# Kernel optimization log

Measured on AMD Instinct MI355X. Metric: run time of the kernel, lower is better.

Reference implementation:

```python
import jax, jax.numpy as jnp
import numpy as np

NUM_HEADS = 8
WEIGHTS_DIM = 512
INPUT_DIM = 512
D_HEAD = WEIGHTS_DIM // NUM_HEADS


def setup_inputs() -> dict:
    key = jax.random.key(0)
    ks = jax.random.split(key, 9)
    B, S, D = 4, 2048, INPUT_DIM
    s_in = 1.0 / np.sqrt(D)
    s_w = 1.0 / np.sqrt(WEIGHTS_DIM)
    return {
        "x": jax.random.normal(ks[0], (B, S, D), dtype=jnp.float32),
        "Wq": jax.random.normal(ks[1], (D, WEIGHTS_DIM), dtype=jnp.float32) * s_in,
        "bq": jnp.zeros((WEIGHTS_DIM,), dtype=jnp.float32),
        "Wk": jax.random.normal(ks[2], (D, WEIGHTS_DIM), dtype=jnp.float32) * s_in,
        "bk": jnp.zeros((WEIGHTS_DIM,), dtype=jnp.float32),
        "Wv": jax.random.normal(ks[3], (D, WEIGHTS_DIM), dtype=jnp.float32) * s_in,
        "bv": jnp.zeros((WEIGHTS_DIM,), dtype=jnp.float32),
        "Wh": jax.random.normal(ks[4], (WEIGHTS_DIM, D), dtype=jnp.float32) * s_w,
        "bh": jnp.zeros((D,), dtype=jnp.float32),
    }


def _split_heads(t):
    # [B, S, Dm] -> [B, H, S, d_head]
    B, S, _ = t.shape
    return t.reshape(B, S, NUM_HEADS, D_HEAD).transpose(0, 2, 1, 3)


def reference(x, Wq, bq, Wk, bk, Wv, bv, Wh, bh):
    q = _split_heads(x @ Wq + bq)
    k = _split_heads(x @ Wk + bk)
    v = _split_heads(x @ Wv + bv)
    scale = 1.0 / jnp.sqrt(jnp.float32(D_HEAD))
    scores = jnp.einsum("bhqd,bhkd->bhqk", q, k) * scale  # [B,H,S,S]
    weights = jax.nn.softmax(scores, axis=-1)
    attn = jnp.einsum("bhqk,bhkd->bhqd", weights, v)
    B, H, S, d = attn.shape
    concat = attn.transpose(0, 2, 1, 3).reshape(B, S, H * d)
    return concat @ Wh + bh
```

## Files before the change

kernel.cpp:

```cpp
#include <hip/hip_runtime.h>
#include <stdint.h>

#define NB  4
#define SS  2048
#define DD  512
#define HH  8
#define DHH 64
#define MM  (NB * SS)

typedef __attribute__((ext_vector_type(8))) short bf16x8;
typedef __attribute__((ext_vector_type(4))) float f32x4;
typedef __attribute__((ext_vector_type(4))) short s16x4;

union fu32 { float f; unsigned u; };
union pfu  { uint4 u; bf16x8 v; };

static __device__ __forceinline__ short f2bf(float f) {
  fu32 a; a.f = f;
  unsigned u = a.u;
  return (short)((u + 0x7fffu + ((u >> 16) & 1u)) >> 16);
}
static __device__ __forceinline__ float bf2f(short s) {
  fu32 t; t.u = ((unsigned)(unsigned short)s) << 16;
  return t.f;
}

static __device__ __forceinline__ void async16(const void* g, void* l) {
  __builtin_amdgcn_global_load_lds(
      (__attribute__((address_space(1))) unsigned*)(void*)g,
      (__attribute__((address_space(3))) unsigned*)l, 16, 0, 0);
}

__global__ __launch_bounds__(256) void prep_kernel(
    const float* __restrict__ x, short* __restrict__ xb,
    const float* __restrict__ W0, const float* __restrict__ W1,
    const float* __restrict__ W2, const float* __restrict__ W3,
    short* __restrict__ T0, short* __restrict__ T1,
    short* __restrict__ T2, short* __restrict__ T3) {
  const int bid = blockIdx.x, tid = threadIdx.x;
  if (bid < 2048) {
    int i = (bid * 256 + tid) * 8;
    float4 v0 = *(const float4*)(x + i);
    float4 v1 = *(const float4*)(x + i + 4);
    bf16x8 o;
    o[0] = f2bf(v0.x); o[1] = f2bf(v0.y); o[2] = f2bf(v0.z); o[3] = f2bf(v0.w);
    o[4] = f2bf(v1.x); o[5] = f2bf(v1.y); o[6] = f2bf(v1.z); o[7] = f2bf(v1.w);
    *(bf16x8*)(xb + i) = o;
  } else {
    int z = bid - 2048;
    int widx = z >> 6, rem = z & 63;
    const float* W = widx == 0 ? W0 : widx == 1 ? W1 : widx == 2 ? W2 : W3;
    short*       T = widx == 0 ? T0 : widx == 1 ? T1 : widx == 2 ? T2 : T3;
    int n  = (rem & 7) * 64 + (tid & 63);
    int k0 = (rem >> 3) * 64 + (tid >> 6) * 16;
    bf16x8 t0, t1;
#pragma unroll
    for (int j = 0; j < 8; ++j) t0[j] = f2bf(W[(size_t)(k0 + j) * DD + n]);
#pragma unroll
    for (int j = 0; j < 8; ++j) t1[j] = f2bf(W[(size_t)(k0 + 8 + j) * DD + n]);
    *(bf16x8*)(T + (size_t)n * DD + k0)     = t0;
    *(bf16x8*)(T + (size_t)n * DD + k0 + 8) = t1;
  }
}

__global__ __launch_bounds__(256, 4) void gemm_qkv_kernel(
    const short* __restrict__ A, const short* __restrict__ Bt,
    const float* __restrict__ bq, const float* __restrict__ bk,
    const float* __restrict__ bv, short* __restrict__ qout,
    short* __restrict__ kout, short* __restrict__ vtout, float qscale) {
  __shared__ __align__(16) short a_sh[64 * 64];
  __shared__ __align__(16) short b_sh[128 * 64];
  const int tid  = threadIdx.x;
  const int w    = tid >> 6, lane = tid & 63, quad = lane >> 4, l16 = lane & 15;
  const int m0   = blockIdx.y * 64, n0 = blockIdx.x * 128;
  const int mw   = (w >> 1) * 32,   nw = (w & 1) * 64;
  const int rw   = lane >> 3, seg = lane & 7, gs = seg ^ rw;
  const int sxz  = l16 & 7;

  f32x4 acc[2][4];
#pragma unroll
  for (int i = 0; i < 2; ++i)
#pragma unroll
    for (int j = 0; j < 4; ++j) acc[i][j] = {0.f, 0.f, 0.f, 0.f};

  for (int kt = 0; kt < DD; kt += 64) {
    __syncthreads();
    {
      const short* ga = A  + (size_t)(m0 + w * 16 + rw) * DD + kt + gs * 8;
      const short* gb = Bt + (size_t)(n0 + w * 32 + rw) * DD + kt + gs * 8;
#pragma unroll
      for (int i = 0; i < 2; ++i)
        async16(ga + (size_t)i * 8 * DD, &a_sh[(w * 16 + i * 8) * 64]);
#pragma unroll
      for (int i = 0; i < 4; ++i)
        async16(gb + (size_t)i * 8 * DD, &b_sh[(w * 32 + i * 8) * 64]);
    }
    __syncthreads();
#pragma unroll
    for (int ks = 0; ks < 2; ++ks) {
      const int so = ((ks * 4 + quad) ^ sxz) * 8;
      bf16x8 af[2], bfr[4];
#pragma unroll
      for (int mt = 0; mt < 2; ++mt)
        af[mt] = *(const bf16x8*)&a_sh[(mw + mt * 16 + l16) * 64 + so];
#pragma unroll
      for (int nt = 0; nt < 4; ++nt)
        bfr[nt] = *(const bf16x8*)&b_sh[(nw + nt * 16 + l16) * 64 + so];
#pragma unroll
      for (int mt = 0; mt < 2; ++mt)
#pragma unroll
        for (int nt = 0; nt < 4; ++nt)
          acc[mt][nt] = __builtin_amdgcn_mfma_f32_16x16x32_bf16(
              af[mt], bfr[nt], acc[mt][nt], 0, 0, 0);
    }
  }

#pragma unroll
  for (int nt = 0; nt < 4; ++nt) {
    const int n   = n0 + nw + nt * 16 + l16;
    const int sg  = n >> 9, n9 = n & 511, h = n9 >> 6, d = n & 63;
    const float bval = (sg == 0 ? bq : sg == 1 ? bk : bv)[n9];
    const float scl  = (sg == 0) ? qscale : 1.0f;
#pragma unroll
    for (int mt = 0; mt < 2; ++mt) {
      const int mb = m0 + mw + mt * 16 + quad * 4;
      const int bi = mb >> 11, s = mb & (SS - 1);
      if (sg == 2) {
        s16x4 pk;
#pragma unroll
        for (int r = 0; r < 4; ++r) pk[r] = f2bf(acc[mt][nt][r] + bval);
        *(s16x4*)&vtout[((size_t)(bi * HH + h) * DHH + d) * SS + s] = pk;
      } else {
        short* o = (sg == 0) ? qout : kout;
        const size_t base = ((size_t)(bi * HH + h) * SS + s) * DHH + d;
#pragma unroll
        for (int r = 0; r < 4; ++r)
          o[base + (size_t)r * DHH] = f2bf((acc[mt][nt][r] + bval) * scl);
      }
    }
  }
}

__global__ __launch_bounds__(256, 4) void attn_kernel(
    const short* __restrict__ Qa, const short* __restrict__ Ka,
    const short* __restrict__ Vt, short* __restrict__ Op0,
    short* __restrict__ Op1, float* __restrict__ lpw) {
  __shared__ __align__(16) short k_sh[128 * 64];
  __shared__ __align__(16) short vt_sh[64 * 128];

  const int tid  = threadIdx.x;
  const int w    = tid >> 6, lane = tid & 63, quad = lane >> 4, l16 = lane & 15;
  const int n    = blockIdx.x;
  const int grp  = (n & 7) * 8 + (n >> 7);
  const int qt_b = (n >> 3) & 15;
  const int half = grp & 1, h = (grp >> 1) & 7, b = grp >> 4;
  const int q0   = qt_b * 128;
  const int rw = lane >> 3, seg = lane & 7, gs = seg ^ rw;
  const int sxz = l16 & 7;
  const size_t base = (size_t)(b * HH + h) * SS * DHH;
  const short* Qg = Qa + base + (size_t)(q0 + w * 32) * DHH;
  const short* Kg = Ka + base;
  const short* Vg = Vt + base;

  bf16x8 qf[2][2];
#pragma unroll
  for (int mt = 0; mt < 2; ++mt)
#pragma unroll
    for (int ks = 0; ks < 2; ++ks)
      qf[mt][ks] = *(const bf16x8*)(Qg + (size_t)(mt * 16 + l16) * DHH + ks * 32 + quad * 8);

  bf16x8 ones;
#pragma unroll
  for (int j = 0; j < 8; ++j) ones[j] = (short)0x3F80;

  f32x4 o_acc[2][4];
#pragma unroll
  for (int qt = 0; qt < 2; ++qt)
#pragma unroll
    for (int dt = 0; dt < 4; ++dt) o_acc[qt][dt] = {0.f, 0.f, 0.f, 0.f};
  f32x4 l_acc[2] = {{0.f, 0.f, 0.f, 0.f}, {0.f, 0.f, 0.f, 0.f}};

  const int addrA = ((((quad & 1) << 1) + (quad >> 1)) * 16 + l16) * 4;
  const int addrB = addrA ^ 64;
  const bool qeven = (quad & 1) == 0;

  const int kstart = half * (SS / 2);

  for (int kb = kstart; kb < kstart + SS / 2; kb += 128) {
    __syncthreads();
    {
      const short* gk = Kg + (size_t)(kb + w * 32 + rw) * DHH + gs * 8;
#pragma unroll
      for (int i = 0; i < 4; ++i)
        async16(gk + (size_t)i * 8 * DHH, &k_sh[(w * 32 + i * 8) * 64]);
#pragma unroll
      for (int i = 0; i < 4; ++i) {
        const int d = w * 16 + i * 4 + (lane >> 4);
        const int gseg = (lane & 15) ^ (d & 15);
        async16(Vg + (size_t)d * SS + kb + gseg * 8,
                &vt_sh[(w * 16 + i * 4) * 128]);
      }
    }
    __syncthreads();

#pragma unroll
    for (int ck = 0; ck < 4; ++ck) {
      uint2 pk[2][2];
#pragma unroll
      for (int t = 0; t < 2; ++t) {
        const int knt = ck * 2 + t;
        bf16x8 kf0 = *(const bf16x8*)&k_sh[(knt * 16 + l16) * 64 + ((0 * 4 + quad) ^ sxz) * 8];
        bf16x8 kf1 = *(const bf16x8*)&k_sh[(knt * 16 + l16) * 64 + ((1 * 4 + quad) ^ sxz) * 8];
#pragma unroll
        for (int qt = 0; qt < 2; ++qt) {
          f32x4 s = {0.f, 0.f, 0.f, 0.f};
          s = __builtin_amdgcn_mfma_f32_16x16x32_bf16(kf0, qf[qt][0], s, 0, 0, 0);
          s = __builtin_amdgcn_mfma_f32_16x16x32_bf16(kf1, qf[qt][1], s, 0, 0, 0);
          fu32 e0, e1, e2, e3;
          e0.f = __builtin_amdgcn_exp2f(s[0]);
          e1.f = __builtin_amdgcn_exp2f(s[1]);
          e2.f = __builtin_amdgcn_exp2f(s[2]);
          e3.f = __builtin_amdgcn_exp2f(s[3]);
          pk[qt][t].x = __builtin_amdgcn_perm(e1.u, e0.u, 0x07060302u);
          pk[qt][t].y = __builtin_amdgcn_perm(e3.u, e2.u, 0x07060302u);
        }
      }
      pfu pf[2];
#pragma unroll
      for (int qt = 0; qt < 2; ++qt) {
        unsigned p1x = (unsigned)__shfl_xor((int)pk[qt][1].x, 16);
        unsigned p1y = (unsigned)__shfl_xor((int)pk[qt][1].y, 16);
        unsigned v0x = qeven ? pk[qt][0].x : p1x;
        unsigned v0y = qeven ? pk[qt][0].y : p1y;
        unsigned v2x = qeven ? p1x : pk[qt][0].x;
        unsigned v2y = qeven ? p1y : pk[qt][0].y;
        pf[qt].u.x = (unsigned)__builtin_amdgcn_ds_bpermute(addrA, (int)v0x);
        pf[qt].u.y = (unsigned)__builtin_amdgcn_ds_bpermute(addrA, (int)v0y);
        pf[qt].u.z = (unsigned)__builtin_amdgcn_ds_bpermute(addrB, (int)v2x);
        pf[qt].u.w = (unsigned)__builtin_amdgcn_ds_bpermute(addrB, (int)v2y);
        l_acc[qt] = __builtin_amdgcn_mfma_f32_16x16x32_bf16(pf[qt].v, ones, l_acc[qt], 0, 0, 0);
      }
#pragma unroll
      for (int dt = 0; dt < 4; ++dt) {
        bf16x8 vf = *(const bf16x8*)&vt_sh[(dt * 16 + l16) * 128 + ((ck * 4 + quad) ^ l16) * 8];
        o_acc[0][dt] = __builtin_amdgcn_mfma_f32_16x16x32_bf16(pf[0].v, vf, o_acc[0][dt], 0, 0, 0);
        o_acc[1][dt] = __builtin_amdgcn_mfma_f32_16x16x32_bf16(pf[1].v, vf, o_acc[1][dt], 0, 0, 0);
      }
    }
  }

  short* Op = half ? Op1 : Op0;
#pragma unroll
  for (int qt = 0; qt < 2; ++qt) {
#pragma unroll
    for (int r = 0; r < 4; ++r) {
      const int qg = q0 + w * 32 + qt * 16 + quad * 4 + r;
      const size_t row = (size_t)(b * HH + h) * SS + qg;
      if (l16 == 0)
        lpw[(size_t)half * (NB * HH * SS) + row] = l_acc[qt][r];
      const float inv = __builtin_amdgcn_rcpf(l_acc[qt][r]);
#pragma unroll
      for (int dt = 0; dt < 4; ++dt)
        Op[row * DHH + dt * 16 + l16] = f2bf(o_acc[qt][dt][r] * inv);
    }
  }
}

__global__ void attn_combine_kernel(const short* __restrict__ Op0,
                                    const short* __restrict__ Op1,
                                    const float* __restrict__ lpw,
                                    short* __restrict__ aws) {
  int idx  = blockIdx.x * 256 + threadIdx.x;
  int dsg  = idx & 7;
  int row  = idx >> 3;
  int q    = row & (SS - 1);
  int bh   = row >> 11, h = bh & 7, b = bh >> 3;
  float l1 = lpw[row], l2 = lpw[NB * HH * SS + row];
  float inv = 1.f / (l1 + l2);
  float w1 = l1 * inv, w2 = l2 * inv;
  bf16x8 a = *(const bf16x8*)&Op0[(size_t)row * DHH + dsg * 8];
  bf16x8 c = *(const bf16x8*)&Op1[(size_t)row * DHH + dsg * 8];
  bf16x8 o;
#pragma unroll
  for (int j = 0; j < 8; ++j) o[j] = f2bf(w1 * bf2f(a[j]) + w2 * bf2f(c[j]));
  *(bf16x8*)&aws[((size_t)(b * SS + q)) * DD + h * DHH + dsg * 8] = o;
}

__global__ __launch_bounds__(256, 4) void gemm_proj_kernel(
    const short* __restrict__ A, const short* __restrict__ Bt,
    const float* __restrict__ bias, float* __restrict__ out) {
  __shared__ __align__(16) short a_sh[64 * 64];
  __shared__ __align__(16) short b_sh[64 * 64];
  const int tid = threadIdx.x;
  const int w   = tid >> 6, lane = tid & 63, quad = lane >> 4, l16 = lane & 15;
  const int m0  = blockIdx.y * 64, n0 = blockIdx.x * 64;
  const int mw  = (w >> 1) * 32, nw = (w & 1) * 32;
  const int rw  = lane >> 3, seg = lane & 7, gs = seg ^ rw;
  const int sxz = l16 & 7;

  f32x4 acc[2][2];
#pragma unroll
  for (int i = 0; i < 2; ++i)
#pragma unroll
    for (int j = 0; j < 2; ++j) acc[i][j] = {0.f, 0.f, 0.f, 0.f};

  for (int kt = 0; kt < DD; kt += 64) {
    __syncthreads();
    {
      const short* ga = A  + (size_t)(m0 + w * 16 + rw) * DD + kt + gs * 8;
      const short* gb = Bt + (size_t)(n0 + w * 16 + rw) * DD + kt + gs * 8;
#pragma unroll
      for (int i = 0; i < 2; ++i) {
        async16(ga + (size_t)i * 8 * DD, &a_sh[(w * 16 + i * 8) * 64]);
        async16(gb + (size_t)i * 8 * DD, &b_sh[(w * 16 + i * 8) * 64]);
      }
    }
    __syncthreads();
#pragma unroll
    for (int ks = 0; ks < 2; ++ks) {
      const int so = ((ks * 4 + quad) ^ sxz) * 8;
      bf16x8 af0 = *(const bf16x8*)&a_sh[(mw + l16) * 64 + so];
      bf16x8 af1 = *(const bf16x8*)&a_sh[(mw + 16 + l16) * 64 + so];
#pragma unroll
      for (int nt = 0; nt < 2; ++nt) {
        bf16x8 bfr = *(const bf16x8*)&b_sh[(nw + nt * 16 + l16) * 64 + so];
        acc[0][nt] = __builtin_amdgcn_mfma_f32_16x16x32_bf16(af0, bfr, acc[0][nt], 0, 0, 0);
        acc[1][nt] = __builtin_amdgcn_mfma_f32_16x16x32_bf16(af1, bfr, acc[1][nt], 0, 0, 0);
      }
    }
  }

#pragma unroll
  for (int nt = 0; nt < 2; ++nt) {
    const int   n  = n0 + nw + nt * 16 + l16;
    const float bv = bias[n];
#pragma unroll
    for (int mt = 0; mt < 2; ++mt)
#pragma unroll
      for (int r = 0; r < 4; ++r) {
        const int m = m0 + mw + mt * 16 + quad * 4 + r;
        out[(size_t)m * DD + n] = acc[mt][nt][r] + bv;
      }
  }
}

extern "C" void kernel_launch(void* const* d_in, const int* in_sizes, int n_in,
                              void* d_out, int out_size, void* d_ws, size_t ws_size,
                              hipStream_t stream) {
  (void)in_sizes; (void)n_in; (void)out_size; (void)ws_size;
  const float* x  = (const float*)d_in[0];
  const float* Wq = (const float*)d_in[1];
  const float* bq = (const float*)d_in[2];
  const float* Wk = (const float*)d_in[3];
  const float* bk = (const float*)d_in[4];
  const float* Wv = (const float*)d_in[5];
  const float* bv = (const float*)d_in[6];
  const float* Wh = (const float*)d_in[7];
  const float* bh = (const float*)d_in[8];

  short* ws  = (short*)d_ws;
  short* xb  = ws;
  short* wqt = xb  + (size_t)MM * DD;
  short* wkt = wqt + (size_t)DD * DD;
  short* wvt = wkt + (size_t)DD * DD;
  short* wht = wvt + (size_t)DD * DD;
  short* qws = wht + (size_t)DD * DD;
  short* kws = qws + (size_t)MM * DD;
  short* vws = kws + (size_t)MM * DD;
  short* aws = vws + (size_t)MM * DD;
  short* op1 = aws + (size_t)MM * DD;
  float* lpw = (float*)(op1 + (size_t)MM * DD);

  hipLaunchKernelGGL(prep_kernel, dim3(2048 + 256), dim3(256), 0, stream,
                     x, xb, Wq, Wk, Wv, Wh, wqt, wkt, wvt, wht);

  const float qscale = 1.4426950408889634f / 8.0f;
  hipLaunchKernelGGL(gemm_qkv_kernel, dim3(12, 128), dim3(256), 0, stream,
                     xb, wqt, bq, bk, bv, qws, kws, vws, qscale);

  hipLaunchKernelGGL(attn_kernel, dim3(1024), dim3(256), 0, stream,
                     qws, kws, vws, xb, op1, lpw);
  hipLaunchKernelGGL(attn_combine_kernel, dim3(NB * HH * SS * 8 / 256), dim3(256), 0, stream,
                     xb, op1, lpw, aws);

  hipLaunchKernelGGL(gemm_proj_kernel, dim3(8, 128), dim3(256), 0, stream,
                     aws, wht, bh, (float*)d_out);
}
```

Before: 176.1 us.

## Enlarge QKV GEMM tile and register-prefetch K/V tiles in attention

The QKV projection GEMM now uses 128x128 block tiles instead of 64x128, so each warp computes a 64x64 sub-tile. This halves the grid and increases reuse of each loaded A/B fragment, at the cost of more accumulator registers and a lower occupancy bound. The attention kernel replaces the async global-to-LDS copies with register prefetch of the next K/V tile, issued while the current tile is being computed, then stored to LDS at the top of the next iteration. This overlaps global memory latency with the MFMA work but raises register pressure.

```diff
diff --git a/kernel.cpp b/kernel.cpp
--- a/kernel.cpp
+++ b/kernel.cpp
@@ -63,34 +63,34 @@
   }
 }
 
-__global__ __launch_bounds__(256, 4) void gemm_qkv_kernel(
+__global__ __launch_bounds__(256, 3) void gemm_qkv_kernel(
     const short* __restrict__ A, const short* __restrict__ Bt,
     const float* __restrict__ bq, const float* __restrict__ bk,
     const float* __restrict__ bv, short* __restrict__ qout,
     short* __restrict__ kout, short* __restrict__ vtout, float qscale) {
-  __shared__ __align__(16) short a_sh[64 * 64];
+  __shared__ __align__(16) short a_sh[128 * 64];
   __shared__ __align__(16) short b_sh[128 * 64];
   const int tid  = threadIdx.x;
   const int w    = tid >> 6, lane = tid & 63, quad = lane >> 4, l16 = lane & 15;
-  const int m0   = blockIdx.y * 64, n0 = blockIdx.x * 128;
-  const int mw   = (w >> 1) * 32,   nw = (w & 1) * 64;
+  const int m0   = blockIdx.y * 128, n0 = blockIdx.x * 128;
+  const int mw   = (w >> 1) * 64,    nw = (w & 1) * 64;
   const int rw   = lane >> 3, seg = lane & 7, gs = seg ^ rw;
   const int sxz  = l16 & 7;
 
-  f32x4 acc[2][4];
-#pragma unroll
-  for (int i = 0; i < 2; ++i)
+  f32x4 acc[4][4];
+#pragma unroll
+  for (int i = 0; i < 4; ++i)
 #pragma unroll
     for (int j = 0; j < 4; ++j) acc[i][j] = {0.f, 0.f, 0.f, 0.f};
 
   for (int kt = 0; kt < DD; kt += 64) {
     __syncthreads();
     {
-      const short* ga = A  + (size_t)(m0 + w * 16 + rw) * DD + kt + gs * 8;
+      const short* ga = A  + (size_t)(m0 + w * 32 + rw) * DD + kt + gs * 8;
       const short* gb = Bt + (size_t)(n0 + w * 32 + rw) * DD + kt + gs * 8;
 #pragma unroll
-      for (int i = 0; i < 2; ++i)
-        async16(ga + (size_t)i * 8 * DD, &a_sh[(w * 16 + i * 8) * 64]);
+      for (int i = 0; i < 4; ++i)
+        async16(ga + (size_t)i * 8 * DD, &a_sh[(w * 32 + i * 8) * 64]);
 #pragma unroll
       for (int i = 0; i < 4; ++i)
         async16(gb + (size_t)i * 8 * DD, &b_sh[(w * 32 + i * 8) * 64]);
@@ -99,15 +99,15 @@
 #pragma unroll
     for (int ks = 0; ks < 2; ++ks) {
       const int so = ((ks * 4 + quad) ^ sxz) * 8;
-      bf16x8 af[2], bfr[4];
-#pragma unroll
-      for (int mt = 0; mt < 2; ++mt)
+      bf16x8 af[4], bfr[4];
+#pragma unroll
+      for (int mt = 0; mt < 4; ++mt)
         af[mt] = *(const bf16x8*)&a_sh[(mw + mt * 16 + l16) * 64 + so];
 #pragma unroll
       for (int nt = 0; nt < 4; ++nt)
         bfr[nt] = *(const bf16x8*)&b_sh[(nw + nt * 16 + l16) * 64 + so];
 #pragma unroll
-      for (int mt = 0; mt < 2; ++mt)
+      for (int mt = 0; mt < 4; ++mt)
 #pragma unroll
         for (int nt = 0; nt < 4; ++nt)
           acc[mt][nt] = __builtin_amdgcn_mfma_f32_16x16x32_bf16(
@@ -122,7 +122,7 @@
     const float bval = (sg == 0 ? bq : sg == 1 ? bk : bv)[n9];
     const float scl  = (sg == 0) ? qscale : 1.0f;
 #pragma unroll
-    for (int mt = 0; mt < 2; ++mt) {
+    for (int mt = 0; mt < 4; ++mt) {
       const int mb = m0 + mw + mt * 16 + quad * 4;
       const int bi = mb >> 11, s = mb & (SS - 1);
       if (sg == 2) {
@@ -185,23 +185,42 @@
   const bool qeven = (quad & 1) == 0;
 
   const int kstart = half * (SS / 2);
-
-  for (int kb = kstart; kb < kstart + SS / 2; kb += 128) {
-    __syncthreads();
-    {
-      const short* gk = Kg + (size_t)(kb + w * 32 + rw) * DHH + gs * 8;
+  const int kend   = kstart + SS / 2;
+
+  const int vd0   = w * 16 + (lane >> 4);
+  uint4 kr[4], vr[4];
+#pragma unroll
+  for (int i = 0; i < 4; ++i)
+    kr[i] = *(const uint4*)(Kg + (size_t)(kstart + w * 32 + i * 8 + rw) * DHH + gs * 8);
+#pragma unroll
+  for (int i = 0; i < 4; ++i) {
+    const int d = vd0 + i * 4;
+    const int gseg = l16 ^ (d & 15);
+    vr[i] = *(const uint4*)(Vg + (size_t)d * SS + kstart + gseg * 8);
+  }
+
+  for (int kb = kstart; kb < kend; kb += 128) {
+    __syncthreads();
+#pragma unroll
+    for (int i = 0; i < 4; ++i)
+      *(uint4*)((char*)&k_sh[(w * 32 + i * 8) * 64] + lane * 16) = kr[i];
+#pragma unroll
+    for (int i = 0; i < 4; ++i)
+      *(uint4*)((char*)&vt_sh[(w * 16 + i * 4) * 128] + lane * 16) = vr[i];
+    __syncthreads();
+
+    if (kb + 128 < kend) {
+      const int nkb = kb + 128;
 #pragma unroll
       for (int i = 0; i < 4; ++i)
-        async16(gk + (size_t)i * 8 * DHH, &k_sh[(w * 32 + i * 8) * 64]);
+        kr[i] = *(const uint4*)(Kg + (size_t)(nkb + w * 32 + i * 8 + rw) * DHH + gs * 8);
 #pragma unroll
       for (int i = 0; i < 4; ++i) {
-        const int d = w * 16 + i * 4 + (lane >> 4);
-        const int gseg = (lane & 15) ^ (d & 15);
-        async16(Vg + (size_t)d * SS + kb + gseg * 8,
-                &vt_sh[(w * 16 + i * 4) * 128]);
-      }
-    }
-    __syncthreads();
+        const int d = vd0 + i * 4;
+        const int gseg = l16 ^ (d & 15);
+        vr[i] = *(const uint4*)(Vg + (size_t)d * SS + nkb + gseg * 8);
+      }
+    }
 
 #pragma unroll
     for (int ck = 0; ck < 4; ++ck) {
@@ -375,7 +394,7 @@
                      x, xb, Wq, Wk, Wv, Wh, wqt, wkt, wvt, wht);
 
   const float qscale = 1.4426950408889634f / 8.0f;
-  hipLaunchKernelGGL(gemm_qkv_kernel, dim3(12, 128), dim3(256), 0, stream,
+  hipLaunchKernelGGL(gemm_qkv_kernel, dim3(12, 64), dim3(256), 0, stream,
                      xb, wqt, bq, bk, bv, qws, kws, vws, qscale);
 
   hipLaunchKernelGGL(attn_kernel, dim3(1024), dim3(256), 0, stream,
```

After: 231.7 us. +31.6%, slower.

## Double-buffer K/V tiles in attention kernel with 64-key stages

Applied to the files above, without the earlier changes.

Replaces the single 128-key K/Vt shared-memory tile with two 64-key buffers, so the async copy of the next tile is issued before computing on the current one. This removes one barrier per iteration and lets global loads overlap with the MFMA work. The tile is halved, so there are twice as many iterations, and the V swizzle changes to match the narrower layout. Total LDS use stays the same.

```diff
diff --git a/kernel.cpp b/kernel.cpp
--- a/kernel.cpp
+++ b/kernel.cpp
@@ -145,8 +145,8 @@
     const short* __restrict__ Qa, const short* __restrict__ Ka,
     const short* __restrict__ Vt, short* __restrict__ Op0,
     short* __restrict__ Op1, float* __restrict__ lpw) {
-  __shared__ __align__(16) short k_sh[128 * 64];
-  __shared__ __align__(16) short vt_sh[64 * 128];
+  __shared__ __align__(16) short k_sh[2][64 * 64];
+  __shared__ __align__(16) short vt_sh[2][64 * 64];
 
   const int tid  = threadIdx.x;
   const int w    = tid >> 6, lane = tid & 63, quad = lane >> 4, l16 = lane & 15;
@@ -185,32 +185,36 @@
   const bool qeven = (quad & 1) == 0;
 
   const int kstart = half * (SS / 2);
-
-  for (int kb = kstart; kb < kstart + SS / 2; kb += 128) {
-    __syncthreads();
-    {
-      const short* gk = Kg + (size_t)(kb + w * 32 + rw) * DHH + gs * 8;
-#pragma unroll
-      for (int i = 0; i < 4; ++i)
-        async16(gk + (size_t)i * 8 * DHH, &k_sh[(w * 32 + i * 8) * 64]);
-#pragma unroll
-      for (int i = 0; i < 4; ++i) {
-        const int d = w * 16 + i * 4 + (lane >> 4);
-        const int gseg = (lane & 15) ^ (d & 15);
-        async16(Vg + (size_t)d * SS + kb + gseg * 8,
-                &vt_sh[(w * 16 + i * 4) * 128]);
-      }
-    }
-    __syncthreads();
-
-#pragma unroll
-    for (int ck = 0; ck < 4; ++ck) {
+  const int kend   = kstart + SS / 2;
+
+  auto stage = [&](int bsel, int kb) {
+    const short* gk = Kg + (size_t)(kb + w * 16 + rw) * DHH + gs * 8;
+#pragma unroll
+    for (int i = 0; i < 2; ++i)
+      async16(gk + (size_t)i * 8 * DHH, &k_sh[bsel][(w * 16 + i * 8) * 64]);
+#pragma unroll
+    for (int i = 0; i < 2; ++i) {
+      const int d = w * 16 + i * 8 + rw;
+      async16(Vg + (size_t)d * SS + kb + gs * 8,
+              &vt_sh[bsel][(w * 16 + i * 8) * 64]);
+    }
+  };
+
+  stage(0, kstart);
+  __syncthreads();
+  int cur = 0;
+
+  for (int kb = kstart; kb < kend; kb += 64) {
+    if (kb + 64 < kend) stage(cur ^ 1, kb + 64);
+
+#pragma unroll
+    for (int ck = 0; ck < 2; ++ck) {
       uint2 pk[2][2];
 #pragma unroll
       for (int t = 0; t < 2; ++t) {
         const int knt = ck * 2 + t;
-        bf16x8 kf0 = *(const bf16x8*)&k_sh[(knt * 16 + l16) * 64 + ((0 * 4 + quad) ^ sxz) * 8];
-        bf16x8 kf1 = *(const bf16x8*)&k_sh[(knt * 16 + l16) * 64 + ((1 * 4 + quad) ^ sxz) * 8];
+        bf16x8 kf0 = *(const bf16x8*)&k_sh[cur][(knt * 16 + l16) * 64 + ((0 * 4 + quad) ^ sxz) * 8];
+        bf16x8 kf1 = *(const bf16x8*)&k_sh[cur][(knt * 16 + l16) * 64 + ((1 * 4 + quad) ^ sxz) * 8];
 #pragma unroll
         for (int qt = 0; qt < 2; ++qt) {
           f32x4 s = {0.f, 0.f, 0.f, 0.f};
@@ -242,11 +246,14 @@
       }
 #pragma unroll
       for (int dt = 0; dt < 4; ++dt) {
-        bf16x8 vf = *(const bf16x8*)&vt_sh[(dt * 16 + l16) * 128 + ((ck * 4 + quad) ^ l16) * 8];
+        bf16x8 vf = *(const bf16x8*)&vt_sh[cur][(dt * 16 + l16) * 64 + ((ck * 4 + quad) ^ sxz) * 8];
         o_acc[0][dt] = __builtin_amdgcn_mfma_f32_16x16x32_bf16(pf[0].v, vf, o_acc[0][dt], 0, 0, 0);
         o_acc[1][dt] = __builtin_amdgcn_mfma_f32_16x16x32_bf16(pf[1].v, vf, o_acc[1][dt], 0, 0, 0);
       }
     }
+
+    __syncthreads();
+    cur ^= 1;
   }
 
   short* Op = half ? Op1 : Op0;
```

New measurement: 178.2 us. No clear change (+1.2%).
